# Kernel tuning notes

Hardware: AMD Instinct MI355X
Metric: run time of the kernel (lower is better)

The kernel has to match this reference:

```python
import jax, jax.numpy as jnp
import numpy as np

B, N, K = 4096, 87, 87


def setup_inputs() -> dict:
    key = jax.random.key(0)
    ks = jax.random.split(key, 6)
    x = jax.random.normal(ks[0], (B, N, N), dtype=jnp.float32)
    evals = jax.random.uniform(ks[1], (B, K), dtype=jnp.float32)
    evecs = jax.random.normal(ks[2], (B, N, K), dtype=jnp.float32)
    # learned per-node diffusion times (torch inits to 0, clamped to 1e-8;
    # use small positive values to exercise the exp decay)
    diffusion_time = jax.random.uniform(ks[3], (N,), dtype=jnp.float32) * 0.1
    # MiniMLP: single Linear(2*N -> N)
    lim = 1.0 / np.sqrt(2 * N)
    W = jax.random.uniform(ks[4], (N, 2 * N), minval=-lim, maxval=lim, dtype=jnp.float32)
    b = jax.random.uniform(ks[5], (N,), minval=-lim, maxval=lim, dtype=jnp.float32)
    return {"x": x, "evals": evals, "evecs": evecs,
            "diffusion_time": diffusion_time, "W": W, "b": b}


def reference(x, evals, evecs, diffusion_time, W, b):
    # clamp diffusion times (torch does this in-place on .data)
    t = jnp.maximum(diffusion_time, 1e-8)                     # (N,)
    # expa[b,i,m] = exp(-t_i * eval[b,m])
    expa = jnp.exp(-t[None, :, None] * evals[:, None, :])     # (B,N,K)
    # kernel[b,i,j] = sum_m evec[b,i,m] * expa[b,i,m] * evec[b,j,m]
    # (equivalent to the diag_embed + triple matmul + diagonal in the torch code)
    kernel = jnp.einsum('bim,bjm->bij', evecs * expa, evecs)  # (B,N,N)
    x_diffuse = jnp.concatenate([x, kernel], axis=2)          # (B,N,2N)
    return x_diffuse @ W.T + b                                # (B,N,N)
```

## Files before the change

### kernel.cpp

```cpp
#include <hip/hip_runtime.h>
#include <hip/hip_bf16.h>
#include <math.h>

#define NN    87
#define NN2   (NN * NN)
#define EPW   92
#define EF1   (NN * EPW + 8)
#define SDN   (NN * EPW + 4)
#define WPH   104
#define WPANEL (96 * WPH)
#define NT    256
#define GRIDB 512

#define PAD_N    8360
#define WS_W     0
#define WS_EPAD  (2 * WPANEL * 2)
#define WS_XPAD  (WS_EPAD + PAD_N * 4)
#define WS_NEED  (WS_XPAD + PAD_N * 4)

typedef __attribute__((ext_vector_type(8))) short bf16x8;
typedef __attribute__((ext_vector_type(4))) short bf16x4;
typedef __attribute__((ext_vector_type(4))) float f32x4;
typedef float f32x4u __attribute__((ext_vector_type(4), aligned(4)));

__device__ __forceinline__ short f2bf(float f) {
    __hip_bfloat16 h = __float2bfloat16(f);
    return *(short*)&h;
}

__device__ __forceinline__ void gl16(const float* g, float* l) {
    __builtin_amdgcn_global_load_lds(
        (const __attribute__((address_space(1))) void*)g,
        (__attribute__((address_space(3))) void*)l, 16, 0, 0);
}

__global__ void prep(const float* __restrict__ W, const float* __restrict__ evecs,
                     const float* __restrict__ x, int B, char* __restrict__ ws)
{
    int idx = (int)blockIdx.x * NT + (int)threadIdx.x;
    short* wpp = (short*)(ws + WS_W);
    float* ep  = (float*)(ws + WS_EPAD);
    float* xp  = (float*)(ws + WS_XPAD);
    if (idx < 2 * WPANEL) {
        int p = idx / WPANEL, rem = idx - p * WPANEL;
        int r = rem / WPH, c = rem - r * WPH;
        short v = 0;
        if (r < NN && c < NN) v = f2bf(W[r * (2 * NN) + p * NN + c]);
        wpp[idx] = v;
    }
    int i2 = idx - 2 * WPANEL;
    if (i2 >= 0 && i2 < PAD_N) ep[i2] = (i2 < NN2) ? evecs[(size_t)(B - 1) * NN2 + i2] : 0.f;
    int i3 = i2 - PAD_N;
    if (i3 >= 0 && i3 < PAD_N) xp[i3] = (i3 < NN2) ? x[(size_t)(B - 1) * NN2 + i3] : 0.f;
}

template <bool WS>
__device__ __forceinline__ bf16x8 wload(const short* __restrict__ wp,
                                        const float* __restrict__ gW,
                                        int panel, int jrow, int jcl, int k0, bool tailKs)
{
    if constexpr (WS) {
        return *(const bf16x8*)&wp[panel * WPANEL + jrow * WPH + k0];
    } else {
        float v[8];
        if (!tailKs) {
            f32x4u a  = *(const f32x4u*)(gW + jcl * (2 * NN) + panel * NN + k0);
            f32x4u b4 = *(const f32x4u*)(gW + jcl * (2 * NN) + panel * NN + k0 + 4);
            v[0] = a.x; v[1] = a.y; v[2] = a.z; v[3] = a.w;
            v[4] = b4.x; v[5] = b4.y; v[6] = b4.z; v[7] = b4.w;
        } else {
            #pragma unroll
            for (int q = 0; q < 8; ++q) {
                int k = k0 + q;
                v[q] = (k < NN) ? gW[jcl * (2 * NN) + panel * NN + k] : 0.f;
            }
        }
        bf16x8 o;
        #pragma unroll
        for (int q = 0; q < 8; ++q) o[q] = f2bf(v[q]);
        return o;
    }
}

template <bool WS>
__device__ __forceinline__ void stageE(const float* __restrict__ Eb, float* __restrict__ sEb,
                                       int tid, int wave, int lane)
{
    if constexpr (WS) {
        for (int vc = wave; vc < 32; vc += 4) {
            int p   = vc * 256 + lane * 4;
            int row = p / EPW;
            int col = p - row * EPW;
            const float* g = Eb + row * NN + col;
            if (vc < 31) gl16(g, &sEb[vc * 256]);
            else if (lane < 17) gl16(g, &sEb[vc * 256]);
        }
    } else {
        for (int u = tid; u < NN * 22; u += NT) {
            int r = u / 22, sg = u - r * 22, c = sg * 4;
            const float* pE = Eb + r * NN + c;
            if (sg < 21) *(f32x4*)&sEb[r * EPW + c] = *(const f32x4u*)pE;
            else { f32x4 t; t.x = pE[0]; t.y = pE[1]; t.z = pE[2]; t.w = 0.f;
                   *(f32x4*)&sEb[r * EPW + c] = t; }
        }
        for (int u = tid; u < NN * 4; u += NT) {
            int r = u >> 2, c = 88 + (u & 3);
            sEb[r * EPW + c] = 0.f;
        }
    }
}

template <bool WS>
__global__ __launch_bounds__(NT, 2)
void fused(const float* __restrict__ gx, const float* __restrict__ gevals,
           const float* __restrict__ gevecs, const float* __restrict__ dtime,
           const float* __restrict__ gW, const float* __restrict__ bias,
           const char* __restrict__ ws, int B, int gridB, float* __restrict__ out)
{
    __shared__ __align__(16) float sE[2][EF1];
    __shared__ __align__(16) short sD[SDN];
    __shared__ float sLam[2][96];

    const int tid  = (int)threadIdx.x;
    const int lane = tid & 63;
    const int wave = tid >> 6;
    const int l15  = lane & 15;
    const int lk   = lane >> 4;
    const int i0   = (wave >> 1) * 48;
    const int j0   = (wave & 1) * 48;

    const short* wp   = nullptr;
    const float* epad = nullptr;
    const float* xpad = nullptr;
    if constexpr (WS) {
        wp   = (const short*)(ws + WS_W);
        epad = (const float*)(ws + WS_EPAD);
        xpad = (const float*)(ws + WS_XPAD);
    }

    int iw[3], jw[3], iru[3], jru[3];
    float tr_[3];
    #pragma unroll
    for (int r = 0; r < 3; ++r) {
        iw[r]  = i0 + 16 * r + l15;
        jw[r]  = j0 + 16 * r + l15;
        iru[r] = (iw[r] < NN) ? iw[r] : NN - 1;
        jru[r] = (jw[r] < NN) ? jw[r] : NN - 1;
        tr_[r] = fmaxf(dtime[iru[r]], 1e-8f);
    }

    bf16x8 wfx[3][3], wfd[3][3];
    #pragma unroll
    for (int ks = 0; ks < 3; ++ks)
        #pragma unroll
        for (int wr = 0; wr < 3; ++wr) {
            wfx[ks][wr] = wload<WS>(wp, gW, 0, jw[wr], jru[wr], ks * 32 + lk * 8, ks == 2);
            wfd[ks][wr] = wload<WS>(wp, gW, 1, jw[wr], jru[wr], ks * 32 + lk * 8, ks == 2);
        }
    float bjv[3][4];
    #pragma unroll
    for (int wr = 0; wr < 3; ++wr) {
        const int jb = j0 + 16 * wr + lk * 4;
        if (jb + 3 < NN) {
            f32x4u t = *(const f32x4u*)(bias + jb);
            bjv[wr][0] = t.x; bjv[wr][1] = t.y; bjv[wr][2] = t.z; bjv[wr][3] = t.w;
        } else {
            #pragma unroll
            for (int q = 0; q < 4; ++q) bjv[wr][q] = (jb + q < NN) ? bias[jb + q] : 0.f;
        }
    }

    if (tid < 8) { sE[0][NN * EPW + tid] = 0.f; sE[1][NN * EPW + tid] = 0.f; }
    if (tid < 4) sD[NN * EPW + tid] = 0;

    const int b0 = (int)blockIdx.x;
    {
        const float* Eb = gevecs + (size_t)b0 * NN2;
        if (WS && b0 == B - 1) Eb = epad;
        stageE<WS>(Eb, sE[0], tid, wave, lane);
        if (tid < 96) sLam[0][tid] = (tid < NN) ? gevals[(size_t)b0 * NN + tid] : 3e38f;
    }
    __syncthreads();

    for (int it = 0, b = b0; b < B; ++it, b += gridB) {
        const int  p  = it & 1;
        const int  bn = b + gridB;
        const bool hn = bn < B;

        const float* xbb = gx + (size_t)b * NN2;
        bool xvec = true;
        if (b == B - 1) { if (WS) xbb = xpad; else xvec = false; }
        float xr[3][3][8];
        #pragma unroll
        for (int xc = 0; xc < 3; ++xc)
            #pragma unroll
            for (int ks = 0; ks < 3; ++ks) {
                const int off = iru[xc] * NN + ks * 32 + lk * 8;
                if (xvec) {
                    f32x4u a  = *(const f32x4u*)(xbb + off);
                    f32x4u b4 = *(const f32x4u*)(xbb + off + 4);
                    xr[xc][ks][0] = a.x;  xr[xc][ks][1] = a.y;
                    xr[xc][ks][2] = a.z;  xr[xc][ks][3] = a.w;
                    xr[xc][ks][4] = b4.x; xr[xc][ks][5] = b4.y;
                    xr[xc][ks][6] = b4.z; xr[xc][ks][7] = b4.w;
                } else {
                    #pragma unroll
                    for (int q = 0; q < 8; ++q) {
                        int o = off + q;
                        xr[xc][ks][q] = xbb[(o < NN2) ? o : (NN2 - 1)];
                    }
                }
            }
        float lamn = 3e38f;
        if (hn && tid < NN) lamn = gevals[(size_t)bn * NN + tid];
        __builtin_amdgcn_sched_barrier(0);

        if (hn) {
            const float* Ebn = gevecs + (size_t)bn * NN2;
            if (WS && bn == B - 1) Ebn = epad;
            stageE<WS>(Ebn, sE[1 - p], tid, wave, lane);
        }

        f32x4 acc1[3][3];
        #pragma unroll
        for (int c = 0; c < 3; ++c)
            #pragma unroll
            for (int r = 0; r < 3; ++r) acc1[c][r] = (f32x4){0.f, 0.f, 0.f, 0.f};

        const float* sEp = sE[p];
        #pragma unroll
        for (int ks = 0; ks < 3; ++ks) {
            const int k0 = ks * 32 + lk * 8;
            f32x4 la  = *(const f32x4*)&sLam[p][k0];
            f32x4 lb4 = *(const f32x4*)&sLam[p][k0 + 4];
            float l8_[8] = {la.x, la.y, la.z, la.w, lb4.x, lb4.y, lb4.z, lb4.w};

            bf16x8 ef[3], af[3];
            #pragma unroll
            for (int c = 0; c < 3; ++c) {
                f32x4 lo = *(const f32x4*)&sEp[jru[c] * EPW + k0];
                f32x4 hi = *(const f32x4*)&sEp[jru[c] * EPW + k0 + 4];
                #pragma unroll
                for (int q = 0; q < 4; ++q) { ef[c][q] = f2bf(lo[q]); ef[c][q + 4] = f2bf(hi[q]); }
            }
            #pragma unroll
            for (int r = 0; r < 3; ++r) {
                f32x4 lo = *(const f32x4*)&sEp[iru[r] * EPW + k0];
                f32x4 hi = *(const f32x4*)&sEp[iru[r] * EPW + k0 + 4];
                #pragma unroll
                for (int q = 0; q < 4; ++q) {
                    af[r][q]     = f2bf(lo[q] * __expf(-tr_[r] * l8_[q]));
                    af[r][q + 4] = f2bf(hi[q] * __expf(-tr_[r] * l8_[q + 4]));
                }
            }
            #pragma unroll
            for (int c = 0; c < 3; ++c)
                #pragma unroll
                for (int r = 0; r < 3; ++r)
                    acc1[c][r] = __builtin_amdgcn_mfma_f32_16x16x32_bf16(ef[c], af[r], acc1[c][r], 0, 0, 0);
        }

        #pragma unroll
        for (int c = 0; c < 3; ++c) {
            const int jb = j0 + 16 * c + lk * 4;
            if (jb < EPW) {
                #pragma unroll
                for (int r = 0; r < 3; ++r) {
                    if (iw[r] < NN) {
                        bf16x4 v = {f2bf(acc1[c][r][0]), f2bf(acc1[c][r][1]),
                                    f2bf(acc1[c][r][2]), f2bf(acc1[c][r][3])};
                        *(bf16x4*)&sD[iw[r] * EPW + jb] = v;
                    }
                }
            }
        }
        if (hn && tid < 96) sLam[1 - p][tid] = (tid < NN) ? lamn : 3e38f;

        asm volatile("s_waitcnt lgkmcnt(0)" ::: "memory");
        __builtin_amdgcn_s_barrier();
        __builtin_amdgcn_sched_barrier(0);

        f32x4 acc2[3][3];
        #pragma unroll
        for (int wr = 0; wr < 3; ++wr)
            #pragma unroll
            for (int xc = 0; xc < 3; ++xc) {
                acc2[wr][xc][0] = bjv[wr][0]; acc2[wr][xc][1] = bjv[wr][1];
                acc2[wr][xc][2] = bjv[wr][2]; acc2[wr][xc][3] = bjv[wr][3];
            }

        #pragma unroll
        for (int ks = 0; ks < 3; ++ks) {
            const int k0 = ks * 32 + lk * 8;
            bf16x8 df[3];
            #pragma unroll
            for (int xc = 0; xc < 3; ++xc) {
                bf16x4 lo = *(const bf16x4*)&sD[iru[xc] * EPW + k0];
                bf16x4 hi = *(const bf16x4*)&sD[iru[xc] * EPW + k0 + 4];
                #pragma unroll
                for (int q = 0; q < 4; ++q) { df[xc][q] = lo[q]; df[xc][q + 4] = hi[q]; }
            }
            #pragma unroll
            for (int wr = 0; wr < 3; ++wr)
                #pragma unroll
                for (int xc = 0; xc < 3; ++xc)
                    acc2[wr][xc] = __builtin_amdgcn_mfma_f32_16x16x32_bf16(
                        wfd[ks][wr], df[xc], acc2[wr][xc], 0, 0, 0);
        }
        #pragma unroll
        for (int ks = 0; ks < 3; ++ks) {
            bf16x8 xf[3];
            #pragma unroll
            for (int xc = 0; xc < 3; ++xc)
                #pragma unroll
                for (int q = 0; q < 8; ++q) xf[xc][q] = f2bf(xr[xc][ks][q]);
            #pragma unroll
            for (int wr = 0; wr < 3; ++wr)
                #pragma unroll
                for (int xc = 0; xc < 3; ++xc)
                    acc2[wr][xc] = __builtin_amdgcn_mfma_f32_16x16x32_bf16(
                        wfx[ks][wr], xf[xc], acc2[wr][xc], 0, 0, 0);
        }

        {
            float* __restrict__ gb = out + (size_t)b * NN2;
            #pragma unroll
            for (int wr = 0; wr < 3; ++wr) {
                const int jb = j0 + 16 * wr + lk * 4;
                #pragma unroll
                for (int xc = 0; xc < 3; ++xc) {
                    const int i = iw[xc];
                    if (i < NN) {
                        if (jb + 3 < NN) {
                            f32x4u v;
                            v.x = acc2[wr][xc][0]; v.y = acc2[wr][xc][1];
                            v.z = acc2[wr][xc][2]; v.w = acc2[wr][xc][3];
                            *(f32x4u*)&gb[i * NN + jb] = v;
                        } else {
                            #pragma unroll
                            for (int q = 0; q < 4; ++q)
                                if (jb + q < NN) gb[i * NN + jb + q] = acc2[wr][xc][q];
                        }
                    }
                }
            }
        }

        if (hn) __syncthreads();
    }
}

extern "C" void kernel_launch(void* const* d_in, const int* in_sizes, int n_in,
                              void* d_out, int out_size, void* d_ws, size_t ws_size,
                              hipStream_t stream)
{
    const float* x     = (const float*)d_in[0];
    const float* evals = (const float*)d_in[1];
    const float* evecs = (const float*)d_in[2];
    const float* dtime = (const float*)d_in[3];
    const float* W     = (const float*)d_in[4];
    const float* bias  = (const float*)d_in[5];
    float* out = (float*)d_out;

    const int B = in_sizes[1] / NN;
    const int gridB = (B < GRIDB) ? B : GRIDB;

    if (ws_size >= (size_t)WS_NEED) {
        const int prep_elems = 2 * WPANEL + 2 * PAD_N;
        prep<<<(prep_elems + NT - 1) / NT, NT, 0, stream>>>(W, evecs, x, B, (char*)d_ws);
        fused<true><<<dim3(gridB), dim3(NT), 0, stream>>>(x, evals, evecs, dtime, W, bias,
                                                          (const char*)d_ws, B, gridB, out);
    } else {
        fused<false><<<dim3(gridB), dim3(NT), 0, stream>>>(x, evals, evecs, dtime, W, bias,
                                                           nullptr, B, gridB, out);
    }
}
```

Baseline: 102.0 us.

## Precompute scaled eigenvector operand once per batch into shared memory

Before, each wave recomputed exp(-t_i*lambda_m) times the eigenvector for its A-operand fragments, so the same exponentials were evaluated redundantly across the waves that share rows. Now all threads cooperatively compute the scaled bf16 matrix once into shared memory (aliasing the sD buffer), separated by a barrier, and the MFMA loop just loads it. The x-term MFMAs are also reordered ahead of the diffusion-term MFMAs, and the next-batch prefetch is moved earlier. This adds an extra block-wide barrier per batch and reuses sD, which needs a second barrier before sD is overwritten.

```diff
diff --git a/kernel.cpp b/kernel.cpp
--- a/kernel.cpp
+++ b/kernel.cpp
@@ -120,6 +120,9 @@
     __shared__ __align__(16) float sE[2][EF1];
     __shared__ __align__(16) short sD[SDN];
     __shared__ float sLam[2][96];
+    __shared__ float sT[88];
+
+    short* const sA = sD;
 
     const int tid  = (int)threadIdx.x;
     const int lane = tid & 63;
@@ -139,14 +142,12 @@
     }
 
     int iw[3], jw[3], iru[3], jru[3];
-    float tr_[3];
     #pragma unroll
     for (int r = 0; r < 3; ++r) {
         iw[r]  = i0 + 16 * r + l15;
         jw[r]  = j0 + 16 * r + l15;
         iru[r] = (iw[r] < NN) ? iw[r] : NN - 1;
         jru[r] = (jw[r] < NN) ? jw[r] : NN - 1;
-        tr_[r] = fmaxf(dtime[iru[r]], 1e-8f);
     }
 
     bf16x8 wfx[3][3], wfd[3][3];
@@ -172,6 +173,7 @@
 
     if (tid < 8) { sE[0][NN * EPW + tid] = 0.f; sE[1][NN * EPW + tid] = 0.f; }
     if (tid < 4) sD[NN * EPW + tid] = 0;
+    if (tid < NN) sT[tid] = fmaxf(dtime[tid], 1e-8f);
 
     const int b0 = (int)blockIdx.x;
     {
@@ -186,6 +188,72 @@
         const int  p  = it & 1;
         const int  bn = b + gridB;
         const bool hn = bn < B;
+
+        if (hn) {
+            const float* Ebn = gevecs + (size_t)bn * NN2;
+            if (WS && bn == B - 1) Ebn = epad;
+            stageE<WS>(Ebn, sE[1 - p], tid, wave, lane);
+        }
+        float lamn = 3e38f;
+        if (hn && tid < NN) lamn = gevals[(size_t)bn * NN + tid];
+
+        const float* sEp = sE[p];
+
+        #pragma unroll
+        for (int m = 0; m < 8; ++m) {
+            const int q4 = tid + m * NT;
+            if (q4 < 2001) {
+                const int off = q4 * 4;
+                const int i = off / EPW;
+                const int k = off - i * EPW;
+                f32x4 ev = *(const f32x4*)&sEp[off];
+                const float t = sT[i];
+                bf16x4 v;
+                v[0] = f2bf(ev.x * __expf(-t * sLam[p][k]));
+                v[1] = f2bf(ev.y * __expf(-t * sLam[p][k + 1]));
+                v[2] = f2bf(ev.z * __expf(-t * sLam[p][k + 2]));
+                v[3] = f2bf(ev.w * __expf(-t * sLam[p][k + 3]));
+                *(bf16x4*)&sA[off] = v;
+            }
+        }
+
+        asm volatile("s_waitcnt lgkmcnt(0)" ::: "memory");
+        __builtin_amdgcn_s_barrier();
+        __builtin_amdgcn_sched_barrier(0);
+
+        f32x4 acc1[3][3];
+        #pragma unroll
+        for (int c = 0; c < 3; ++c)
+            #pragma unroll
+            for (int r = 0; r < 3; ++r) acc1[c][r] = (f32x4){0.f, 0.f, 0.f, 0.f};
+
+        #pragma unroll
+        for (int ks = 0; ks < 3; ++ks) {
+            const int k0 = ks * 32 + lk * 8;
+            bf16x8 ef[3], af[3];
+            #pragma unroll
+            for (int c = 0; c < 3; ++c) {
+                f32x4 lo = *(const f32x4*)&sEp[jru[c] * EPW + k0];
+                f32x4 hi = *(const f32x4*)&sEp[jru[c] * EPW + k0 + 4];
+                #pragma unroll
+                for (int q = 0; q < 4; ++q) { ef[c][q] = f2bf(lo[q]); ef[c][q + 4] = f2bf(hi[q]); }
+            }
+            const bool hiZero = (ks == 2) && (lk == 3);
+            #pragma unroll
+            for (int r = 0; r < 3; ++r) {
+                bf16x4 lo = *(const bf16x4*)&sA[iru[r] * EPW + k0];
+                bf16x4 hi;
+                if (hiZero) hi = (bf16x4){0, 0, 0, 0};
+                else        hi = *(const bf16x4*)&sA[iru[r] * EPW + k0 + 4];
+                #pragma unroll
+                for (int q = 0; q < 4; ++q) { af[r][q] = lo[q]; af[r][q + 4] = hi[q]; }
+            }
+            #pragma unroll
+            for (int c = 0; c < 3; ++c)
+                #pragma unroll
+                for (int r = 0; r < 3; ++r)
+                    acc1[c][r] = __builtin_amdgcn_mfma_f32_16x16x32_bf16(ef[c], af[r], acc1[c][r], 0, 0, 0);
+        }
 
         const float* xbb = gx + (size_t)b * NN2;
         bool xvec = true;
@@ -211,54 +279,10 @@
                     }
                 }
             }
-        float lamn = 3e38f;
-        if (hn && tid < NN) lamn = gevals[(size_t)bn * NN + tid];
+
+        asm volatile("s_waitcnt lgkmcnt(0)" ::: "memory");
+        __builtin_amdgcn_s_barrier();
         __builtin_amdgcn_sched_barrier(0);
-
-        if (hn) {
-            const float* Ebn = gevecs + (size_t)bn * NN2;
-            if (WS && bn == B - 1) Ebn = epad;
-            stageE<WS>(Ebn, sE[1 - p], tid, wave, lane);
-        }
-
-        f32x4 acc1[3][3];
-        #pragma unroll
-        for (int c = 0; c < 3; ++c)
-            #pragma unroll
-            for (int r = 0; r < 3; ++r) acc1[c][r] = (f32x4){0.f, 0.f, 0.f, 0.f};
-
-        const float* sEp = sE[p];
-        #pragma unroll
-        for (int ks = 0; ks < 3; ++ks) {
-            const int k0 = ks * 32 + lk * 8;
-            f32x4 la  = *(const f32x4*)&sLam[p][k0];
-            f32x4 lb4 = *(const f32x4*)&sLam[p][k0 + 4];
-            float l8_[8] = {la.x, la.y, la.z, la.w, lb4.x, lb4.y, lb4.z, lb4.w};
-
-            bf16x8 ef[3], af[3];
-            #pragma unroll
-            for (int c = 0; c < 3; ++c) {
-                f32x4 lo = *(const f32x4*)&sEp[jru[c] * EPW + k0];
-                f32x4 hi = *(const f32x4*)&sEp[jru[c] * EPW + k0 + 4];
-                #pragma unroll
-                for (int q = 0; q < 4; ++q) { ef[c][q] = f2bf(lo[q]); ef[c][q + 4] = f2bf(hi[q]); }
-            }
-            #pragma unroll
-            for (int r = 0; r < 3; ++r) {
-                f32x4 lo = *(const f32x4*)&sEp[iru[r] * EPW + k0];
-                f32x4 hi = *(const f32x4*)&sEp[iru[r] * EPW + k0 + 4];
-                #pragma unroll
-                for (int q = 0; q < 4; ++q) {
-                    af[r][q]     = f2bf(lo[q] * __expf(-tr_[r] * l8_[q]));
-                    af[r][q + 4] = f2bf(hi[q] * __expf(-tr_[r] * l8_[q + 4]));
-                }
-            }
-            #pragma unroll
-            for (int c = 0; c < 3; ++c)
-                #pragma unroll
-                for (int r = 0; r < 3; ++r)
-                    acc1[c][r] = __builtin_amdgcn_mfma_f32_16x16x32_bf16(ef[c], af[r], acc1[c][r], 0, 0, 0);
-        }
 
         #pragma unroll
         for (int c = 0; c < 3; ++c) {
@@ -291,6 +315,20 @@
 
         #pragma unroll
         for (int ks = 0; ks < 3; ++ks) {
+            bf16x8 xf[3];
+            #pragma unroll
+            for (int xc = 0; xc < 3; ++xc)
+                #pragma unroll
+                for (int q = 0; q < 8; ++q) xf[xc][q] = f2bf(xr[xc][ks][q]);
+            #pragma unroll
+            for (int wr = 0; wr < 3; ++wr)
+                #pragma unroll
+                for (int xc = 0; xc < 3; ++xc)
+                    acc2[wr][xc] = __builtin_amdgcn_mfma_f32_16x16x32_bf16(
+                        wfx[ks][wr], xf[xc], acc2[wr][xc], 0, 0, 0);
+        }
+        #pragma unroll
+        for (int ks = 0; ks < 3; ++ks) {
             const int k0 = ks * 32 + lk * 8;
             bf16x8 df[3];
             #pragma unroll
@@ -306,20 +344,6 @@
                 for (int xc = 0; xc < 3; ++xc)
                     acc2[wr][xc] = __builtin_amdgcn_mfma_f32_16x16x32_bf16(
                         wfd[ks][wr], df[xc], acc2[wr][xc], 0, 0, 0);
-        }
-        #pragma unroll
-        for (int ks = 0; ks < 3; ++ks) {
-            bf16x8 xf[3];
-            #pragma unroll
-            for (int xc = 0; xc < 3; ++xc)
-                #pragma unroll
-                for (int q = 0; q < 8; ++q) xf[xc][q] = f2bf(xr[xc][ks][q]);
-            #pragma unroll
-            for (int wr = 0; wr < 3; ++wr)
-                #pragma unroll
-                for (int xc = 0; xc < 3; ++xc)
-                    acc2[wr][xc] = __builtin_amdgcn_mfma_f32_16x16x32_bf16(
-                        wfx[ks][wr], xf[xc], acc2[wr][xc], 0, 0, 0);
         }
 
         {
```

Measured after the change: 88.90 us. 12.8% less time.
